# Kernel optimization log

Hardware: AMD Instinct MI355X
Metric: run time of the kernel (lower is better)

## Reference

```python
import jax, jax.numpy as jnp
import numpy as np

N_HEAD = 8
GROUPS = 16
EPS = 1e-5
C = 256


def group_norm(x, gamma, beta):
    # x: (B, C, H, W); GroupNorm over (C//G, H, W) within each group
    B, Cc, H, W = x.shape
    xg = x.reshape(B, GROUPS, Cc // GROUPS, H * W)
    mu = xg.mean(axis=(2, 3), keepdims=True)
    var = xg.var(axis=(2, 3), keepdims=True)
    xn = ((xg - mu) * jax.lax.rsqrt(var + EPS)).reshape(B, Cc, H, W)
    return xn * gamma[None, :, None, None] + beta[None, :, None, None]


def cross_attn(q, k, v, channel):
    # q, k, v: (B, n_head, head_dim, H, W); full bidirectional spatial attention
    B, n, d, H, W = q.shape
    scores = jnp.einsum('bnchw,bncyx->bnhwyx', q, k) / np.float32(np.sqrt(channel))
    attn = jax.nn.softmax(scores.reshape(B, n, H, W, H * W), axis=-1)
    attn = attn.reshape(B, n, H, W, H, W)
    out = jnp.einsum('bnhwyx,bncyx->bnchw', attn, v)
    return out.reshape(B, n * d, H, W)


def conv1x1(w, x, b=None):
    # w: (Cout, Cin), x: (B, Cin, H, W)
    y = jnp.einsum('oc,bchw->bohw', w, x)
    if b is not None:
        y = y + b[None, :, None, None]
    return y


def setup_inputs() -> dict:
    key = jax.random.key(0)
    ks = jax.random.split(key, 8)
    B, H, W = 16, 32, 32
    s = 1.0 / np.sqrt(C)
    return {
        'x_A': jax.random.normal(ks[0], (B, C, H, W), jnp.float32),
        'x_B': jax.random.normal(ks[1], (B, C, H, W), jnp.float32),
        'gA': jnp.ones((C,), jnp.float32),
        'bA': jnp.zeros((C,), jnp.float32),
        'gB': jnp.ones((C,), jnp.float32),
        'bB': jnp.zeros((C,), jnp.float32),
        'WqkvA': jax.random.normal(ks[2], (3 * C, C), jnp.float32) * s,
        'WqkvB': jax.random.normal(ks[3], (3 * C, C), jnp.float32) * s,
        'WoutA': jax.random.normal(ks[4], (C, C), jnp.float32) * s,
        'boutA': jnp.zeros((C,), jnp.float32),
        'WoutB': jax.random.normal(ks[5], (C, C), jnp.float32) * s,
        'boutB': jnp.zeros((C,), jnp.float32),
    }


def reference(x_A, x_B, gA, bA, gB, bB, WqkvA, WqkvB, WoutA, boutA, WoutB, boutB):
    B, Cc, H, W = x_A.shape
    d = Cc // N_HEAD
    norm_A = group_norm(x_A, gA, bA)
    norm_B = group_norm(x_B, gB, bB)
    qkvA = conv1x1(WqkvA, norm_A).reshape(B, N_HEAD, 3 * d, H, W)
    qA, kA, vA = jnp.split(qkvA, 3, axis=2)
    qkvB = conv1x1(WqkvB, norm_B).reshape(B, N_HEAD, 3 * d, H, W)
    qB, kB, vB = jnp.split(qkvB, 3, axis=2)
    # A branch attends query_B -> key/value_A (note scale uses full channel count)
    out_A = conv1x1(WoutA, cross_attn(qB, kA, vA, Cc), boutA) + norm_A
    out_B = conv1x1(WoutB, cross_attn(qA, kB, vB, Cc), boutB) + norm_B
    return (out_A, out_B)
```

## Files before the change

### kernel.cpp

```cpp
#include <hip/hip_runtime.h>
#include <hip/hip_bf16.h>
#include <math.h>

typedef __attribute__((ext_vector_type(8))) short short8;
typedef __attribute__((ext_vector_type(4))) short short4_;
typedef __attribute__((ext_vector_type(4))) float f32x4;
typedef __attribute__((ext_vector_type(4))) unsigned int uint4_;

#define MFMA16(a, b, c) __builtin_amdgcn_mfma_f32_16x16x32_bf16((a), (b), (c), 0, 0, 0)

#define OFF_XTA   0
#define OFF_XTB   8388608
#define OFF_QBA   16777216
#define OFF_KBA   25165824
#define OFF_VBA   33554432
#define OFF_QBB   41943040
#define OFF_KBB   50331648
#define OFF_VBB   58720256
#define OFF_AOA   67108864
#define OFF_AOB   75497472
#define OFF_WQA   83886080
#define OFF_WQB   84279296
#define OFF_WOA   84672512
#define OFF_WOB   84803584

__device__ __forceinline__ short f2bf(float f) {
  union { float f; unsigned u; } v; v.f = f;
  unsigned r = v.u + 0x7fffu + ((v.u >> 16) & 1u);
  return (short)(r >> 16);
}

__device__ __forceinline__ float bf2f(short s) {
  union { float f; unsigned u; } v; v.u = ((unsigned)(unsigned short)s) << 16;
  return v.f;
}

__device__ __forceinline__ unsigned pk2bf(float a, float b) {
  union { __hip_bfloat162 h2; unsigned u; } cv;
  cv.h2 = __float22bfloat162_rn(float2{a, b});
  return cv.u;
}

__device__ __forceinline__ unsigned pktrunc(float a, float b) {
#if __has_builtin(__builtin_amdgcn_perm)
  return __builtin_amdgcn_perm(__builtin_bit_cast(unsigned, b),
                               __builtin_bit_cast(unsigned, a), 0x07060302u);
#else
  return (__builtin_bit_cast(unsigned, b) & 0xffff0000u) |
         (__builtin_bit_cast(unsigned, a) >> 16);
#endif
}

__device__ __forceinline__ float approx_exp2(float x) {
  int i = (int)__builtin_fmaf(x, 8388608.0f, 1064991921.0f);
  return __builtin_bit_cast(float, i);
}

__device__ __forceinline__ void load_lds16(const void* g, void* l) {
  __builtin_amdgcn_global_load_lds((const __attribute__((address_space(1))) void*)g,
                                   (__attribute__((address_space(3))) void*)l, 16, 0, 0);
}

#define QSCALE 0.09016844005556f

__global__ __launch_bounds__(256) void prep_kernel(const float* __restrict__ xA,
                                                   const float* __restrict__ xB,
                                                   const float* __restrict__ gA,
                                                   const float* __restrict__ bA,
                                                   const float* __restrict__ gB,
                                                   const float* __restrict__ bB,
                                                   const float* __restrict__ wqA,
                                                   const float* __restrict__ wqB,
                                                   const float* __restrict__ woA,
                                                   const float* __restrict__ woB,
                                                   char* __restrict__ ws) {
  const int blk = blockIdx.x;
  const int t = threadIdx.x;
  if (blk >= 512) {
    int wb = blk - 512;
    const float* src; short* dst; int base;
    if (wb < 96) { src = wqA; dst = (short*)(ws + OFF_WQA); base = wb; }
    else if (wb < 192) { src = wqB; dst = (short*)(ws + OFF_WQB); base = wb - 96; }
    else if (wb < 224) { src = woA; dst = (short*)(ws + OFF_WOA); base = wb - 192; }
    else { src = woB; dst = (short*)(ws + OFF_WOB); base = wb - 224; }
    int idx = base * 2048 + t * 8;
    float4 a = *(const float4*)(src + idx);
    float4 b = *(const float4*)(src + idx + 4);
    uint4_ o;
    o[0] = pk2bf(a.x, a.y); o[1] = pk2bf(a.z, a.w);
    o[2] = pk2bf(b.x, b.y); o[3] = pk2bf(b.z, b.w);
    *(uint4_*)(dst + idx) = o;
    return;
  }
  const int br = blk >> 8, sub = blk & 255;
  const int b = sub >> 4, g = sub & 15;
  const float* x = br ? xB : xA;
  const float* gamma = br ? gB : gA;
  const float* beta = br ? bB : bA;
  short* Xt = (short*)(ws + (br ? OFF_XTB : OFF_XTA));
  const size_t base = (size_t)sub * 16384;
  const float4* xp = (const float4*)(x + base);
  float s = 0.f, q = 0.f;
  float4 vals[16];
  for (int i = 0; i < 16; ++i) {
    float4 v = xp[t + i * 256];
    vals[i] = v;
    s += v.x + v.y + v.z + v.w;
    q += v.x * v.x + v.y * v.y + v.z * v.z + v.w * v.w;
  }
  __shared__ float rs[256], rq[256];
  rs[t] = s; rq[t] = q;
  __syncthreads();
  for (int o = 128; o > 0; o >>= 1) {
    if (t < o) { rs[t] += rs[t + o]; rq[t] += rq[t + o]; }
    __syncthreads();
  }
  __shared__ float sh_mu, sh_inv;
  if (t == 0) {
    float mu = rs[0] * (1.f / 16384.f);
    float var = rq[0] * (1.f / 16384.f) - mu * mu;
    sh_mu = mu;
    sh_inv = rsqrtf(var + 1e-5f);
  }
  __syncthreads();
  const float mu = sh_mu, inv = sh_inv;
  unsigned td[4][8];
#pragma unroll
  for (int i = 0; i < 16; i += 2) {
    int c = (g << 4) + i;
    float ga0 = gamma[c] * inv, be0 = beta[c] - mu * ga0;
    float ga1 = gamma[c + 1] * inv, be1 = beta[c + 1] - mu * ga1;
    float4 v0 = vals[i], v1 = vals[i + 1];
    td[0][i >> 1] = pk2bf(v0.x * ga0 + be0, v1.x * ga1 + be1);
    td[1][i >> 1] = pk2bf(v0.y * ga0 + be0, v1.y * ga1 + be1);
    td[2][i >> 1] = pk2bf(v0.z * ga0 + be0, v1.z * ga1 + be1);
    td[3][i >> 1] = pk2bf(v0.w * ga0 + be0, v1.w * ga1 + be1);
  }
  short* orow = Xt + ((size_t)b * 1024 + 4 * t) * 256 + (g << 4);
#pragma unroll
  for (int j = 0; j < 4; ++j) {
    *(uint4_*)(orow + j * 256) = *(const uint4_*)&td[j][0];
    *(uint4_*)(orow + j * 256 + 8) = *(const uint4_*)&td[j][4];
  }
}

__global__ __launch_bounds__(256) void gemm_qkv_kernel(char* __restrict__ ws) {
  const int n0 = blockIdx.x * 128, m0 = blockIdx.y * 128;
  const int b = blockIdx.z & 15, br = blockIdx.z >> 4;
  const short* Wb = (const short*)(ws + (br ? OFF_WQB : OFF_WQA));
  const short* Xt = (const short*)(ws + (br ? OFF_XTB : OFF_XTA));
  short* Qb = (short*)(ws + (br ? OFF_QBB : OFF_QBA));
  short* Kb = Qb + 4194304;
  short* Vb = Qb + 8388608;
  const int t = threadIdx.x;
  __shared__ short As[128 * 64];
  __shared__ short Bs[128 * 64];
  const int w = t >> 6, lane = t & 63, l15 = lane & 15, quad = lane >> 4;
  const int wm = (w >> 1) * 64, wn = (w & 1) * 64;
  const f32x4 z4 = {0.f, 0.f, 0.f, 0.f};
  f32x4 acc[4][4];
  for (int i = 0; i < 4; i++)
    for (int j = 0; j < 4; j++) acc[i][j] = z4;

  const int srow = lane >> 3, cpos = lane & 7;
  const int swz = (cpos ^ srow) * 8;
  const short* wg = Wb + (size_t)(m0 + w * 32 + srow) * 256 + swz;
  const short* xg = Xt + ((size_t)b * 1024 + n0 + w * 32 + srow) * 256 + swz;
  short* lA = &As[(w * 32) * 64];
  short* lB = &Bs[(w * 32) * 64];

  for (int k0 = 0; k0 < 256; k0 += 64) {
    __syncthreads();
#pragma unroll
    for (int qq = 0; qq < 4; ++qq) {
      load_lds16(wg + (size_t)qq * 8 * 256 + k0, lA + qq * 8 * 64);
      load_lds16(xg + (size_t)qq * 8 * 256 + k0, lB + qq * 8 * 64);
    }
    __syncthreads();
#pragma unroll
    for (int s = 0; s < 2; ++s) {
      const int cc = ((s * 4 + quad) ^ (l15 & 7)) * 8;
      short8 af[4], bfb[4];
      for (int i = 0; i < 4; i++) af[i] = *(const short8*)&As[(wm + i * 16 + l15) * 64 + cc];
      for (int j = 0; j < 4; j++) bfb[j] = *(const short8*)&Bs[(wn + j * 16 + l15) * 64 + cc];
      for (int i = 0; i < 4; i++)
        for (int j = 0; j < 4; j++) acc[i][j] = MFMA16(af[i], bfb[j], acc[i][j]);
    }
  }
  for (int i = 0; i < 4; i++) {
    int mi = m0 + wm + i * 16;
    int h = mi / 96;
    int rr = mi - h * 96;
    if (rr < 64) {
      short* dst = (rr < 32) ? Qb : Kb;
      const float mul = (rr < 32) ? QSCALE : 1.0f;
      const int dbase = (rr & 31) + quad * 4;
      const size_t rowb = ((size_t)b * 8 + h) * 1024;
      for (int j = 0; j < 4; j++) {
        int n = n0 + wn + j * 16 + l15;
        union { unsigned u[2]; short4_ s; } uv;
        uv.u[0] = pk2bf(acc[i][j][0] * mul, acc[i][j][1] * mul);
        uv.u[1] = pk2bf(acc[i][j][2] * mul, acc[i][j][3] * mul);
        *(short4_*)(dst + (rowb + n) * 32 + dbase) = uv.s;
      }
    } else {
      const int dv = (rr - 64) + quad * 4;
      const size_t vb = (((size_t)b * 8 + h) * 32 + dv) * 1024;
      for (int j = 0; j < 4; j++) {
        int n = n0 + wn + j * 16 + l15;
        for (int r = 0; r < 4; r++) Vb[vb + (size_t)r * 1024 + n] = f2bf(acc[i][j][r]);
      }
    }
  }
}

__global__ __launch_bounds__(256) void attn_kernel(char* __restrict__ ws) {
  const int b = blockIdx.x, h = blockIdx.y;
  const int qt = blockIdx.z & 3, br = blockIdx.z >> 2;
  const short* Qb = (const short*)(ws + (br ? OFF_QBA : OFF_QBB));
  const short* Kb = (const short*)(ws + (br ? OFF_KBB : OFF_KBA));
  const short* Vb = Kb + 4194304;
  short* AO = (short*)(ws + (br ? OFF_AOB : OFF_AOA));
  const int t = threadIdx.x;
  const int w = t >> 6, lane = t & 63, l15 = lane & 15, quad = lane >> 4;
  const size_t hb = (size_t)(b * 8 + h);
  const f32x4 z4 = {0.f, 0.f, 0.f, 0.f};
  __shared__ short Ks[256 * 32];
  __shared__ short Vs[32 * 256];

  const int q0 = qt * 256 + w * 64;
  short8 bq[4];
#pragma unroll
  for (int s = 0; s < 4; ++s)
    bq[s] = *(const short8*)(Qb + (hb * 1024 + q0 + s * 16 + l15) * 32 + quad * 8);
  const short* Kg = Kb + hb * 1024 * 32;
  const short* Vg = Vb + hb * 32 * 1024;

  short8 ones;
#pragma unroll
  for (int i = 0; i < 8; ++i) ones[i] = (short)0x3F80;

  const int rk_off = lane >> 2;
  const int ck = lane & 3;
  const int rv_off = lane >> 5;
  const int cv = lane & 31;
  const int kread = l15 * 32 + ((quad ^ ((l15 >> 1) & 3)) * 8);

  f32x4 accO[4][2];
  f32x4 accL[4];
#pragma unroll
  for (int s = 0; s < 4; ++s) { accO[s][0] = z4; accO[s][1] = z4; accL[s] = z4; }

  for (int k0 = 0; k0 < 1024; k0 += 256) {
    __syncthreads();
    for (int p = 0; p < 4; ++p) {
      const int rk = (w * 4 + p) * 16 + rk_off;
      load_lds16(Kg + (size_t)(k0 + rk) * 32 + ((ck ^ ((rk >> 1) & 3)) * 8),
                 &Ks[(w * 4 + p) * 512]);
      const int rv = (w * 4 + p) * 2 + rv_off;
      load_lds16(Vg + (size_t)rv * 1024 + k0 + ((cv ^ (rv & 15)) * 8),
                 &Vs[(w * 4 + p) * 512]);
    }
    __syncthreads();

#pragma unroll
    for (int pr = 0; pr < 8; ++pr) {
      const short8 ak0 = *(const short8*)&Ks[(2 * pr) * 512 + kread];
      const short8 ak1 = *(const short8*)&Ks[(2 * pr + 1) * 512 + kread];
      const int cg = pr * 4 + (quad >> 1);
      const int so = (quad & 1) * 4;
      union { short8 s; short4_ hh[2]; } bv[2];
#pragma unroll
      for (int dvt = 0; dvt < 2; ++dvt) {
        const int dvrow = (dvt * 16 + l15) * 256;
        bv[dvt].hh[0] = *(const short4_*)&Vs[dvrow + ((cg ^ l15) * 8) + so];
        bv[dvt].hh[1] = *(const short4_*)&Vs[dvrow + (((cg + 2) ^ l15) * 8) + so];
      }
#pragma unroll
      for (int s = 0; s < 4; ++s) {
        f32x4 st0 = MFMA16(ak0, bq[s], z4);
        f32x4 st1 = MFMA16(ak1, bq[s], z4);
        union { short8 s8; uint4_ u; } apv;
        float p0 = approx_exp2(st0[0]), p1 = approx_exp2(st0[1]);
        float p2 = approx_exp2(st0[2]), p3 = approx_exp2(st0[3]);
        float p4 = approx_exp2(st1[0]), p5 = approx_exp2(st1[1]);
        float p6 = approx_exp2(st1[2]), p7 = approx_exp2(st1[3]);
        apv.u[0] = pktrunc(p0, p1); apv.u[1] = pktrunc(p2, p3);
        apv.u[2] = pktrunc(p4, p5); apv.u[3] = pktrunc(p6, p7);
        accO[s][0] = MFMA16(apv.s8, bv[0].s, accO[s][0]);
        accO[s][1] = MFMA16(apv.s8, bv[1].s, accO[s][1]);
        accL[s] = MFMA16(apv.s8, ones, accL[s]);
      }
    }
  }

#pragma unroll
  for (int s = 0; s < 4; ++s) {
    for (int r = 0; r < 4; r++) {
      float inv = 1.0f / accL[s][r];
      int sq = q0 + s * 16 + quad * 4 + r;
      short* orow = AO + ((size_t)b * 1024 + sq) * 256 + h * 32 + l15;
      orow[0] = f2bf(accO[s][0][r] * inv);
      orow[16] = f2bf(accO[s][1][r] * inv);
    }
  }
}

__global__ __launch_bounds__(256) void gemm_out_kernel(char* __restrict__ ws,
                                                       const float* __restrict__ boutA,
                                                       const float* __restrict__ boutB,
                                                       float* __restrict__ outbase) {
  const int m0 = blockIdx.x * 128, n0 = blockIdx.y * 128;
  const int b = blockIdx.z & 15, br = blockIdx.z >> 4;
  const short* Wob = (const short*)(ws + (br ? OFF_WOB : OFF_WOA));
  const short* ao = (const short*)(ws + (br ? OFF_AOB : OFF_AOA));
  const float* bias = br ? boutB : boutA;
  const short* Xt = (const short*)(ws + (br ? OFF_XTB : OFF_XTA));
  float* out = outbase + (br ? 4194304 : 0);
  const int t = threadIdx.x;
  __shared__ short smem[128 * 64 * 2];
  short* As = smem;
  short* Bs = smem + 128 * 64;
  const int w = t >> 6, lane = t & 63, l15 = lane & 15, quad = lane >> 4;
  const int wm = (w >> 1) * 64, wn = (w & 1) * 64;
  const f32x4 z4 = {0.f, 0.f, 0.f, 0.f};
  f32x4 acc[4][4];
  for (int i = 0; i < 4; i++)
    for (int j = 0; j < 4; j++) acc[i][j] = z4;

  const int srow = lane >> 3, cpos = lane & 7;
  const int swz = (cpos ^ srow) * 8;
  const short* wg = Wob + (size_t)(m0 + w * 32 + srow) * 256 + swz;
  const short* xg = ao + ((size_t)b * 1024 + n0 + w * 32 + srow) * 256 + swz;
  short* lA = &As[(w * 32) * 64];
  short* lB = &Bs[(w * 32) * 64];

  for (int k0 = 0; k0 < 256; k0 += 64) {
    __syncthreads();
#pragma unroll
    for (int qq = 0; qq < 4; ++qq) {
      load_lds16(wg + (size_t)qq * 8 * 256 + k0, lA + qq * 8 * 64);
      load_lds16(xg + (size_t)qq * 8 * 256 + k0, lB + qq * 8 * 64);
    }
    __syncthreads();
#pragma unroll
    for (int s = 0; s < 2; ++s) {
      const int cc = ((s * 4 + quad) ^ (l15 & 7)) * 8;
      short8 af[4], bfb[4];
      for (int i = 0; i < 4; i++) af[i] = *(const short8*)&As[(wm + i * 16 + l15) * 64 + cc];
      for (int j = 0; j < 4; j++) bfb[j] = *(const short8*)&Bs[(wn + j * 16 + l15) * 64 + cc];
      for (int i = 0; i < 4; i++)
        for (int j = 0; j < 4; j++) acc[i][j] = MFMA16(af[i], bfb[j], acc[i][j]);
    }
  }

  __syncthreads();
  {
    const int rrow = lane >> 4, rc = lane & 15;
    for (int qq = 0; qq < 8; ++qq) {
      int row = w * 32 + qq * 4 + rrow;
      load_lds16(Xt + ((size_t)b * 1024 + n0 + row) * 256 + m0 + ((rc ^ (row & 15)) * 8),
                 &smem[(w * 32 + qq * 4) * 128]);
    }
  }
  __syncthreads();

  for (int i = 0; i < 4; i++)
    for (int j = 0; j < 4; j++) {
      int m = m0 + wm + i * 16 + quad * 4;
      int nl = wn + j * 16 + l15;
      int n = n0 + nl;
      size_t off = ((size_t)b * 256 + m) * 1024 + n;
      const int chunk = (wm >> 3) + i * 2 + (quad >> 1);
      short4_ rv = *(const short4_*)&smem[nl * 128 + ((chunk ^ (nl & 15)) * 8) + (quad & 1) * 4];
      for (int r = 0; r < 4; r++)
        out[off + (size_t)r * 1024] = acc[i][j][r] + bias[m + r] + bf2f(rv[r]);
    }
}

extern "C" void kernel_launch(void* const* d_in, const int* in_sizes, int n_in,
                              void* d_out, int out_size, void* d_ws, size_t ws_size,
                              hipStream_t stream) {
  const float* xA = (const float*)d_in[0];
  const float* xB = (const float*)d_in[1];
  const float* gA = (const float*)d_in[2];
  const float* bA = (const float*)d_in[3];
  const float* gB = (const float*)d_in[4];
  const float* bB = (const float*)d_in[5];
  const float* WqkvA = (const float*)d_in[6];
  const float* WqkvB = (const float*)d_in[7];
  const float* WoutA = (const float*)d_in[8];
  const float* boutA = (const float*)d_in[9];
  const float* WoutB = (const float*)d_in[10];
  const float* boutB = (const float*)d_in[11];
  float* out = (float*)d_out;
  char* ws = (char*)d_ws;

  prep_kernel<<<768, 256, 0, stream>>>(xA, xB, gA, bA, gB, bB,
                                       WqkvA, WqkvB, WoutA, WoutB, ws);
  gemm_qkv_kernel<<<dim3(8, 6, 32), 256, 0, stream>>>(ws);
  attn_kernel<<<dim3(16, 8, 8), 256, 0, stream>>>(ws);
  gemm_out_kernel<<<dim3(2, 8, 32), 256, 0, stream>>>(ws, boutA, boutB, out);
}
```

Before: 182.8 us.

## Double-buffer K/V tiles in attention kernel with async prefetch

The attention kernel now splits each 256-key chunk into 128-key tiles held in two LDS buffers. The next tile is prefetched through direct-to-LDS loads while the current tile is computed, with manual vmcnt waits and raw barriers in place of __syncthreads. It also raises wave priority around the MFMA compute section. The aim is to hide global load latency behind the MFMA and exp work. The cost is more barriers per key and hand-written wait counts that must match the number of outstanding loads.

```diff
diff --git a/kernel.cpp b/kernel.cpp
--- a/kernel.cpp
+++ b/kernel.cpp
@@ -225,8 +225,8 @@
   const int w = t >> 6, lane = t & 63, l15 = lane & 15, quad = lane >> 4;
   const size_t hb = (size_t)(b * 8 + h);
   const f32x4 z4 = {0.f, 0.f, 0.f, 0.f};
-  __shared__ short Ks[256 * 32];
-  __shared__ short Vs[32 * 256];
+  __shared__ short Ks[2][128 * 32];
+  __shared__ short Vs[2][32 * 128];
 
   const int q0 = qt * 256 + w * 64;
   short8 bq[4];
@@ -242,8 +242,8 @@
 
   const int rk_off = lane >> 2;
   const int ck = lane & 3;
-  const int rv_off = lane >> 5;
-  const int cv = lane & 31;
+  const int rv_off = lane >> 4;
+  const int cv = lane & 15;
   const int kread = l15 * 32 + ((quad ^ ((l15 >> 1) & 3)) * 8);
 
   f32x4 accO[4][2];
@@ -251,30 +251,34 @@
 #pragma unroll
   for (int s = 0; s < 4; ++s) { accO[s][0] = z4; accO[s][1] = z4; accL[s] = z4; }
 
-  for (int k0 = 0; k0 < 1024; k0 += 256) {
-    __syncthreads();
-    for (int p = 0; p < 4; ++p) {
-      const int rk = (w * 4 + p) * 16 + rk_off;
+  auto STAGE = [&](int c, int tt) {
+    const int k0 = tt * 128;
+#pragma unroll
+    for (int p = 0; p < 2; ++p) {
+      const int rk = (w * 2 + p) * 16 + rk_off;
       load_lds16(Kg + (size_t)(k0 + rk) * 32 + ((ck ^ ((rk >> 1) & 3)) * 8),
-                 &Ks[(w * 4 + p) * 512]);
-      const int rv = (w * 4 + p) * 2 + rv_off;
+                 &Ks[c][(w * 2 + p) * 512]);
+      const int rv = (w * 2 + p) * 4 + rv_off;
       load_lds16(Vg + (size_t)rv * 1024 + k0 + ((cv ^ (rv & 15)) * 8),
-                 &Vs[(w * 4 + p) * 512]);
-    }
-    __syncthreads();
-
-#pragma unroll
-    for (int pr = 0; pr < 8; ++pr) {
-      const short8 ak0 = *(const short8*)&Ks[(2 * pr) * 512 + kread];
-      const short8 ak1 = *(const short8*)&Ks[(2 * pr + 1) * 512 + kread];
+                 &Vs[c][(w * 2 + p) * 512]);
+    }
+  };
+
+  auto COMPUTE = [&](int c) {
+    const short* KsC = &Ks[c][0];
+    const short* VsC = &Vs[c][0];
+#pragma unroll
+    for (int pr = 0; pr < 4; ++pr) {
+      const short8 ak0 = *(const short8*)&KsC[(2 * pr) * 512 + kread];
+      const short8 ak1 = *(const short8*)&KsC[(2 * pr + 1) * 512 + kread];
       const int cg = pr * 4 + (quad >> 1);
       const int so = (quad & 1) * 4;
       union { short8 s; short4_ hh[2]; } bv[2];
 #pragma unroll
       for (int dvt = 0; dvt < 2; ++dvt) {
-        const int dvrow = (dvt * 16 + l15) * 256;
-        bv[dvt].hh[0] = *(const short4_*)&Vs[dvrow + ((cg ^ l15) * 8) + so];
-        bv[dvt].hh[1] = *(const short4_*)&Vs[dvrow + (((cg + 2) ^ l15) * 8) + so];
+        const int dvrow = (dvt * 16 + l15) * 128;
+        bv[dvt].hh[0] = *(const short4_*)&VsC[dvrow + ((cg ^ l15) * 8) + so];
+        bv[dvt].hh[1] = *(const short4_*)&VsC[dvrow + (((cg + 2) ^ l15) * 8) + so];
       }
 #pragma unroll
       for (int s = 0; s < 4; ++s) {
@@ -292,6 +296,25 @@
         accL[s] = MFMA16(apv.s8, ones, accL[s]);
       }
     }
+  };
+
+  STAGE(0, 0);
+#pragma unroll
+  for (int tt = 0; tt < 8; ++tt) {
+    const int c = tt & 1;
+    if (tt < 7) {
+      STAGE(c ^ 1, tt + 1);
+      asm volatile("s_waitcnt vmcnt(4)" ::: "memory");
+    } else {
+      asm volatile("s_waitcnt vmcnt(0)" ::: "memory");
+    }
+    __builtin_amdgcn_s_barrier();
+    __builtin_amdgcn_sched_barrier(0);
+    __builtin_amdgcn_s_setprio(1);
+    COMPUTE(c);
+    __builtin_amdgcn_s_setprio(0);
+    __builtin_amdgcn_sched_barrier(0);
+    __builtin_amdgcn_s_barrier();
   }
 
 #pragma unroll
```

Measured after the change: 189.4 us. 1.04x slower.
